# Performance work log

Hardware: AMD Instinct MI355X
Metric: run time of the kernel (lower is better)

The kernel has to match this reference:

```python
import jax, jax.numpy as jnp
import numpy as np

C = 256
E = C // 2  # embed_dim = in_channels / 2


def setup_inputs() -> dict:
    key = jax.random.key(0)
    ks = jax.random.split(key, 9)
    B, H, W = 8, 64, 64
    x = jax.random.normal(ks[0], (B, C, H, W), dtype=jnp.float32)
    s_in = 1.0 / np.sqrt(C)
    s_e = 1.0 / np.sqrt(E)
    wq = jax.random.uniform(ks[1], (E, C), jnp.float32, -s_in, s_in)
    bq = jax.random.uniform(ks[2], (E,), jnp.float32, -s_in, s_in)
    wk = jax.random.uniform(ks[3], (E, C), jnp.float32, -s_in, s_in)
    bk = jax.random.uniform(ks[4], (E,), jnp.float32, -s_in, s_in)
    wv = jax.random.uniform(ks[5], (E, C), jnp.float32, -s_in, s_in)
    bv = jax.random.uniform(ks[6], (E,), jnp.float32, -s_in, s_in)
    wo = jax.random.uniform(ks[7], (C, E), jnp.float32, -s_e, s_e)
    bo = jax.random.uniform(ks[8], (C,), jnp.float32, -s_e, s_e)
    return {"x": x, "wq": wq, "bq": bq, "wk": wk, "bk": bk,
            "wv": wv, "bv": bv, "wo": wo, "bo": bo}


def reference(x, wq, bq, wk, bk, wv, bv, wo, bo):
    B, Cc, H, W = x.shape
    N = H * W
    # flatten spatial: [B, N, C]; 1x1 conv == per-pixel linear over channels
    xf = x.reshape(B, Cc, N).transpose(0, 2, 1)
    q = jnp.einsum('bnc,ec->bne', xf, wq) + bq   # [B, N, E]
    k = jnp.einsum('bnc,ec->bne', xf, wk) + bk   # [B, N, E]
    v = jnp.einsum('bnc,ec->bne', xf, wv) + bv   # [B, N, E]
    attn_score = jnp.einsum('bne,bme->bnm', q, k)  # [B, N, N]
    attn_prob = jax.nn.softmax(attn_score, axis=-1)
    feat = jnp.einsum('bnm,bme->bne', attn_prob, v)  # [B, N, E]
    out = jnp.einsum('bne,ce->bnc', feat, wo) + bo   # expansion 1x1 conv
    out = out.transpose(0, 2, 1).reshape(B, Cc, H, W)
    return out + x
```

## Files before the change

### kernel.cpp

```cpp
#include <hip/hip_runtime.h>
#include <hip/hip_bf16.h>


typedef __attribute__((ext_vector_type(8))) short s16x8;
typedef __attribute__((ext_vector_type(4))) short s16x4;
typedef __attribute__((ext_vector_type(4))) float f32x4;

#define B_ 8
#define C_ 256
#define E_ 128
#define N_ 4096
#define SHIFT 15.0f

static __device__ __forceinline__ unsigned short f2bf(float f) {
    union { float f; unsigned int u; } v; v.f = f;
    return (unsigned short)((v.u + 0x7FFFu + ((v.u >> 16) & 1u)) >> 16);
}
static __device__ __forceinline__ float bf2f(unsigned short h) {
    union { unsigned int u; float f; } v; v.u = ((unsigned int)h) << 16;
    return v.f;
}

__global__ __launch_bounds__(256) void convert_w(
    const float* __restrict__ wq, const float* __restrict__ wk,
    const float* __restrict__ wv, const float* __restrict__ wo,
    unsigned short* __restrict__ wqb, unsigned short* __restrict__ wkb,
    unsigned short* __restrict__ wvb, unsigned short* __restrict__ wob)
{
    const int i = blockIdx.x * 256 + threadIdx.x;
    wqb[i] = f2bf(wq[i]);
    wkb[i] = f2bf(wk[i]);
    wvb[i] = f2bf(wv[i]);
    wob[i] = f2bf(wo[i]);
}

__global__ __launch_bounds__(256, 2) void qkv_kernel(
    const float* __restrict__ x,
    const unsigned short* __restrict__ wqb, const float* __restrict__ bq,
    const unsigned short* __restrict__ wkb, const float* __restrict__ bk,
    const unsigned short* __restrict__ wvb, const float* __restrict__ bv,
    unsigned short* __restrict__ Q, unsigned short* __restrict__ K,
    unsigned short* __restrict__ Vt)
{
    __shared__ unsigned short xs[64 * 264];

    const int tid = threadIdx.x;
    const int b  = blockIdx.x >> 6;
    const int n0 = (blockIdx.x & 63) << 6;

    {
        const int n  = tid & 63;
        const int c0 = tid >> 6;
        const float* xp = x + ((size_t)(b * C_) << 12) + n0 + n;
        for (int it = 0; it < 64; ++it) {
            const int c = it * 4 + c0;
            xs[n * 264 + c] = f2bf(xp[(size_t)c << 12]);
        }
    }
    __syncthreads();

    const int w = tid >> 6, l = tid & 63, hi = l >> 4, lx = l & 15;

    for (int idx = w; idx < 24; idx += 4) {
        const int out = idx >> 3;
        const int et  = idx & 7;
        const int e0  = et << 4;
        const unsigned short* W = (out == 0) ? wqb : (out == 1) ? wkb : wvb;
        const float* bias = (out == 0) ? bq : (out == 1) ? bk : bv;

        s16x8 af[8];
        const unsigned short* wp = W + (e0 + lx) * C_ + hi * 8;
#pragma unroll
        for (int ks = 0; ks < 8; ++ks) af[ks] = *(const s16x8*)(wp + ks * 32);

        float bi[4];
#pragma unroll
        for (int r = 0; r < 4; ++r) bi[r] = bias[e0 + hi * 4 + r];

#pragma unroll
        for (int nt = 0; nt < 4; ++nt) {
            f32x4 acc = {0.f, 0.f, 0.f, 0.f};
#pragma unroll
            for (int ks = 0; ks < 8; ++ks) {
                s16x8 xb = *(const s16x8*)&xs[(nt * 16 + lx) * 264 + ks * 32 + hi * 8];
                acc = __builtin_amdgcn_mfma_f32_16x16x32_bf16(af[ks], xb, acc, 0, 0, 0);
            }
            const int n = n0 + nt * 16 + lx;
            if (out < 2) {
                unsigned short* dst =
                    ((out == 0) ? Q : K) + ((size_t)(b * N_ + n) << 7) + e0 + hi * 4;
                s16x4 pk;
#pragma unroll
                for (int r = 0; r < 4; ++r) pk[r] = (short)f2bf(acc[r] + bi[r]);
                *(s16x4*)dst = pk;
            } else {
#pragma unroll
                for (int r = 0; r < 4; ++r)
                    Vt[((size_t)(b * E_ + e0 + hi * 4 + r) << 12) + n] =
                        f2bf(acc[r] + bi[r]);
            }
        }
    }
}

__global__ __launch_bounds__(256, 2) void attn_partial(
    const unsigned short* __restrict__ Q, const unsigned short* __restrict__ K,
    const unsigned short* __restrict__ Vt,
    unsigned short* __restrict__ featP, float* __restrict__ denomP)
{
    __shared__ unsigned short Ks[64 * 136];
    __shared__ unsigned short Vs[128 * 72];
    __shared__ unsigned short Ps[4][32 * 72];

    const int tid = threadIdx.x;
    const int b   = blockIdx.x & 7;
    const int idx = blockIdx.x >> 3;
    const int sl  = idx >> 5;
    const int qt  = idx & 31;
    const int w = tid >> 6, l = tid & 63, hi = l >> 4, lx = l & 15;
    const int q0 = qt * 128 + w * 32;

    s16x8 qA[2][4];
#pragma unroll
    for (int qf = 0; qf < 2; ++qf) {
        const unsigned short* qp =
            Q + ((size_t)(b * N_ + q0 + qf * 16 + lx) << 7) + hi * 8;
#pragma unroll
        for (int ks = 0; ks < 4; ++ks) qA[qf][ks] = *(const s16x8*)(qp + ks * 32);
    }

    f32x4 feat[2][8];
#pragma unroll
    for (int qf = 0; qf < 2; ++qf)
#pragma unroll
        for (int ef = 0; ef < 8; ++ef) feat[qf][ef] = (f32x4){0.f, 0.f, 0.f, 0.f};
    float dAcc[8];
#pragma unroll
    for (int i = 0; i < 8; ++i) dAcc[i] = 0.f;

    const unsigned short* Kg = K + ((size_t)(b * N_) << 7);
    const unsigned short* Vg = Vt + ((size_t)(b * E_) << 12);
    const int pswz_w = hi << 3;
    const int pswz_r = (lx & 12) << 1;

    for (int it = 0; it < 16; ++it) {
        const int kv0 = (sl << 10) + it * 64;
        __syncthreads();
#pragma unroll
        for (int i = 0; i < 4; ++i) {
            const int flat = tid + i * 256;
            const int row = flat >> 4, c16 = flat & 15;
            *(s16x8*)&Ks[row * 136 + c16 * 8] =
                *(const s16x8*)(Kg + (size_t)(kv0 + row) * 128 + c16 * 8);
        }
#pragma unroll
        for (int i = 0; i < 4; ++i) {
            const int flat = tid + i * 256;
            const int e = flat >> 3, c16 = flat & 7;
            *(s16x8*)&Vs[e * 72 + c16 * 8] =
                *(const s16x8*)(Vg + ((size_t)e << 12) + kv0 + c16 * 8);
        }
        __syncthreads();

        unsigned short* pw = &Ps[w][0];
#pragma unroll
        for (int kvf = 0; kvf < 4; ++kvf) {
            s16x8 kb[4];
#pragma unroll
            for (int ks = 0; ks < 4; ++ks)
                kb[ks] = *(const s16x8*)&Ks[(kvf * 16 + lx) * 136 + ks * 32 + hi * 8];
            const int pcol = (kvf * 16 + lx) ^ pswz_w;
#pragma unroll
            for (int qf = 0; qf < 2; ++qf) {
                f32x4 acc = {0.f, 0.f, 0.f, 0.f};
#pragma unroll
                for (int ks = 0; ks < 4; ++ks)
                    acc = __builtin_amdgcn_mfma_f32_16x16x32_bf16(qA[qf][ks], kb[ks], acc, 0, 0, 0);
#pragma unroll
                for (int r = 0; r < 4; ++r) {
                    float p = __expf(acc[r] - SHIFT);
                    dAcc[qf * 4 + r] += p;
                    pw[(qf * 16 + hi * 4 + r) * 72 + pcol] = f2bf(p);
                }
            }
        }
#pragma unroll
        for (int ks = 0; ks < 2; ++ks) {
            s16x8 pa[2];
#pragma unroll
            for (int qf = 0; qf < 2; ++qf)
                pa[qf] = *(const s16x8*)&pw[(qf * 16 + lx) * 72 +
                                            ((ks * 32 + hi * 8) ^ pswz_r)];
#pragma unroll
            for (int ef = 0; ef < 8; ++ef) {
                s16x8 vb = *(const s16x8*)&Vs[(ef * 16 + lx) * 72 + ks * 32 + hi * 8];
#pragma unroll
                for (int qf = 0; qf < 2; ++qf)
                    feat[qf][ef] = __builtin_amdgcn_mfma_f32_16x16x32_bf16(pa[qf], vb, feat[qf][ef], 0, 0, 0);
            }
        }
    }

#pragma unroll
    for (int i = 0; i < 8; ++i) {
        float v = dAcc[i];
        v += __shfl_xor(v, 1); v += __shfl_xor(v, 2);
        v += __shfl_xor(v, 4); v += __shfl_xor(v, 8);
        dAcc[i] = v;
    }
    const size_t qg = (size_t)((sl * 8 + b) * N_ + qt * 128 + w * 32);
    if (lx == 0) {
        float* dP = denomP + qg;
#pragma unroll
        for (int qf = 0; qf < 2; ++qf)
#pragma unroll
            for (int r = 0; r < 4; ++r)
                dP[qf * 16 + hi * 4 + r] = dAcc[qf * 4 + r];
    }
    unsigned short* fP = featP + (qg << 7);
#pragma unroll
    for (int qf = 0; qf < 2; ++qf)
#pragma unroll
        for (int ef = 0; ef < 8; ++ef)
#pragma unroll
            for (int r = 0; r < 4; ++r)
                fP[(qf * 16 + hi * 4 + r) * 128 + ef * 16 + lx] =
                    f2bf(feat[qf][ef][r]);
}

__global__ __launch_bounds__(256, 2) void combine_kernel(
    const unsigned short* __restrict__ featP, const float* __restrict__ denomP,
    const unsigned short* __restrict__ wob, const float* __restrict__ bo,
    const float* __restrict__ x, float* __restrict__ out)
{
    __shared__ unsigned short fs[64 * 136];

    const int tid = threadIdx.x;
    const int b  = blockIdx.x & 7;
    const int nt = blockIdx.x >> 3;

    {
        const int q = tid >> 2, eb = (tid & 3) * 32;
        const int n = nt * 64 + q;
        float den = 0.f;
#pragma unroll
        for (int s = 0; s < 4; ++s) den += denomP[(size_t)((s * 8 + b) * N_) + n];
        const float inv = 1.f / den;
#pragma unroll
        for (int e8 = 0; e8 < 4; ++e8) {
            float acc[8];
#pragma unroll
            for (int j = 0; j < 8; ++j) acc[j] = 0.f;
#pragma unroll
            for (int s = 0; s < 4; ++s) {
                s16x8 v = *(const s16x8*)(featP +
                    (((size_t)((s * 8 + b) * N_) + n) << 7) + eb + e8 * 8);
#pragma unroll
                for (int j = 0; j < 8; ++j) acc[j] += bf2f((unsigned short)v[j]);
            }
            s16x8 o;
#pragma unroll
            for (int j = 0; j < 8; ++j) o[j] = (short)f2bf(acc[j] * inv);
            *(s16x8*)&fs[q * 136 + eb + e8 * 8] = o;
        }
    }
    __syncthreads();

    const int w = tid >> 6, l = tid & 63, hi = l >> 4, lx = l & 15;

    s16x8 fa[4];
#pragma unroll
    for (int ks = 0; ks < 4; ++ks)
        fa[ks] = *(const s16x8*)&fs[(w * 16 + lx) * 136 + ks * 32 + hi * 8];

    const int n = nt * 64 + w * 16 + lx;
    const float* xb = x + ((size_t)(b * C_) << 12);
    float* ob = out + ((size_t)(b * C_) << 12);
#pragma unroll 1
    for (int ct = 0; ct < 16; ++ct) {
        const unsigned short* wp = wob + (ct * 16 + lx) * 128 + hi * 8;
        f32x4 acc = {0.f, 0.f, 0.f, 0.f};
#pragma unroll
        for (int ks = 0; ks < 4; ++ks) {
            s16x8 wb = *(const s16x8*)(wp + ks * 32);
            acc = __builtin_amdgcn_mfma_f32_16x16x32_bf16(wb, fa[ks], acc, 0, 0, 0);
        }
#pragma unroll
        for (int r = 0; r < 4; ++r) {
            const int c = ct * 16 + hi * 4 + r;
            const size_t off = ((size_t)c << 12) + n;
            ob[off] = acc[r] + bo[c] + xb[off];
        }
    }
}

extern "C" void kernel_launch(void* const* d_in, const int* in_sizes, int n_in,
                              void* d_out, int out_size, void* d_ws, size_t ws_size,
                              hipStream_t stream) {
    (void)in_sizes; (void)n_in; (void)out_size; (void)ws_size;
    const float* x  = (const float*)d_in[0];
    const float* wq = (const float*)d_in[1];
    const float* bq = (const float*)d_in[2];
    const float* wk = (const float*)d_in[3];
    const float* bk = (const float*)d_in[4];
    const float* wv = (const float*)d_in[5];
    const float* bv = (const float*)d_in[6];
    const float* wo = (const float*)d_in[7];
    const float* bo = (const float*)d_in[8];

    unsigned short* Q  = (unsigned short*)d_ws;
    unsigned short* K  = Q + (size_t)B_ * N_ * E_;
    unsigned short* Vt = K + (size_t)B_ * N_ * E_;
    unsigned short* featP = Vt + (size_t)B_ * N_ * E_;
    float* denomP = (float*)(featP + (size_t)4 * B_ * N_ * E_);
    unsigned short* wqb = (unsigned short*)(denomP + (size_t)4 * B_ * N_);
    unsigned short* wkb = wqb + E_ * C_;
    unsigned short* wvb = wkb + E_ * C_;
    unsigned short* wob = wvb + E_ * C_;

    convert_w<<<dim3(128), dim3(256), 0, stream>>>(
        wq, wk, wv, wo, wqb, wkb, wvb, wob);
    qkv_kernel<<<dim3(B_ * (N_ / 64)), dim3(256), 0, stream>>>(
        x, wqb, bq, wkb, bk, wvb, bv, Q, K, Vt);
    attn_partial<<<dim3(B_ * 32 * 4), dim3(256), 0, stream>>>(
        Q, K, Vt, featP, denomP);
    combine_kernel<<<dim3(B_ * 64), dim3(256), 0, stream>>>(
        featP, denomP, wob, bo, x, (float*)d_out);
}
```

Measured before the change: 143.7 us.

## Prefetch next KV tile into registers and halve KV split slices

The attention kernel now loads the next K/V tile from global memory into registers while computing on the current tile in shared memory, overlapping global latency with MFMA work. The number of KV slices is cut from 4 to 2, which halves the partial feat/denominator traffic and combine work but also halves the grid (512 blocks) and doubles per-block loop length. The XOR swizzle on the P scratch buffer is replaced by a padded stride of 76, changing the bank-conflict pattern. Register pressure rises from holding the prefetched tile.

```diff
diff --git a/kernel.cpp b/kernel.cpp
--- a/kernel.cpp
+++ b/kernel.cpp
@@ -10,6 +10,10 @@
 #define C_ 256
 #define E_ 128
 #define N_ 4096
+#define SLICES 2
+#define SLICE_KV (N_ / SLICES)
+#define NT (SLICE_KV / 64)
+#define PST 76
 #define SHIFT 15.0f
 
 static __device__ __forceinline__ unsigned short f2bf(float f) {
@@ -110,7 +114,7 @@
 {
     __shared__ unsigned short Ks[64 * 136];
     __shared__ unsigned short Vs[128 * 72];
-    __shared__ unsigned short Ps[4][32 * 72];
+    __shared__ unsigned short Ps[4][32 * PST];
 
     const int tid = threadIdx.x;
     const int b   = blockIdx.x & 7;
@@ -140,28 +144,32 @@
 
     const unsigned short* Kg = K + ((size_t)(b * N_) << 7);
     const unsigned short* Vg = Vt + ((size_t)(b * E_) << 12);
-    const int pswz_w = hi << 3;
-    const int pswz_r = (lx & 12) << 1;
-
-    for (int it = 0; it < 16; ++it) {
-        const int kv0 = (sl << 10) + it * 64;
-        __syncthreads();
-#pragma unroll
-        for (int i = 0; i < 4; ++i) {
-            const int flat = tid + i * 256;
-            const int row = flat >> 4, c16 = flat & 15;
-            *(s16x8*)&Ks[row * 136 + c16 * 8] =
-                *(const s16x8*)(Kg + (size_t)(kv0 + row) * 128 + c16 * 8);
-        }
-#pragma unroll
-        for (int i = 0; i < 4; ++i) {
-            const int flat = tid + i * 256;
-            const int e = flat >> 3, c16 = flat & 7;
-            *(s16x8*)&Vs[e * 72 + c16 * 8] =
-                *(const s16x8*)(Vg + ((size_t)e << 12) + kv0 + c16 * 8);
-        }
-        __syncthreads();
-
+    const int kvBase = sl * SLICE_KV;
+
+    const int kRow[4] = { (tid + 0) >> 4, (tid + 256) >> 4,
+                          (tid + 512) >> 4, (tid + 768) >> 4 };
+    const int kC16 = tid & 15;
+    const int vE[4]  = { (tid + 0) >> 3, (tid + 256) >> 3,
+                         (tid + 512) >> 3, (tid + 768) >> 3 };
+    const int vC16 = tid & 7;
+
+    auto loadTile = [&](int kv0, s16x8* nk, s16x8* nv) {
+#pragma unroll
+        for (int i = 0; i < 4; ++i)
+            nk[i] = *(const s16x8*)(Kg + (size_t)(kv0 + kRow[i]) * 128 + kC16 * 8);
+#pragma unroll
+        for (int i = 0; i < 4; ++i)
+            nv[i] = *(const s16x8*)(Vg + ((size_t)vE[i] << 12) + kv0 + vC16 * 8);
+    };
+    auto writeTile = [&](const s16x8* nk, const s16x8* nv) {
+#pragma unroll
+        for (int i = 0; i < 4; ++i)
+            *(s16x8*)&Ks[kRow[i] * 136 + kC16 * 8] = nk[i];
+#pragma unroll
+        for (int i = 0; i < 4; ++i)
+            *(s16x8*)&Vs[vE[i] * 72 + vC16 * 8] = nv[i];
+    };
+    auto compute = [&]() {
         unsigned short* pw = &Ps[w][0];
 #pragma unroll
         for (int kvf = 0; kvf < 4; ++kvf) {
@@ -169,7 +177,6 @@
 #pragma unroll
             for (int ks = 0; ks < 4; ++ks)
                 kb[ks] = *(const s16x8*)&Ks[(kvf * 16 + lx) * 136 + ks * 32 + hi * 8];
-            const int pcol = (kvf * 16 + lx) ^ pswz_w;
 #pragma unroll
             for (int qf = 0; qf < 2; ++qf) {
                 f32x4 acc = {0.f, 0.f, 0.f, 0.f};
@@ -180,7 +187,7 @@
                 for (int r = 0; r < 4; ++r) {
                     float p = __expf(acc[r] - SHIFT);
                     dAcc[qf * 4 + r] += p;
-                    pw[(qf * 16 + hi * 4 + r) * 72 + pcol] = f2bf(p);
+                    pw[(qf * 16 + hi * 4 + r) * PST + kvf * 16 + lx] = f2bf(p);
                 }
             }
         }
@@ -189,8 +196,7 @@
             s16x8 pa[2];
 #pragma unroll
             for (int qf = 0; qf < 2; ++qf)
-                pa[qf] = *(const s16x8*)&pw[(qf * 16 + lx) * 72 +
-                                            ((ks * 32 + hi * 8) ^ pswz_r)];
+                pa[qf] = *(const s16x8*)&pw[(qf * 16 + lx) * PST + ks * 32 + hi * 8];
 #pragma unroll
             for (int ef = 0; ef < 8; ++ef) {
                 s16x8 vb = *(const s16x8*)&Vs[(ef * 16 + lx) * 72 + ks * 32 + hi * 8];
@@ -199,7 +205,24 @@
                     feat[qf][ef] = __builtin_amdgcn_mfma_f32_16x16x32_bf16(pa[qf], vb, feat[qf][ef], 0, 0, 0);
             }
         }
-    }
+    };
+
+    {
+        s16x8 nk[4], nv[4];
+        loadTile(kvBase, nk, nv);
+        writeTile(nk, nv);
+    }
+    __syncthreads();
+
+    for (int it = 0; it < NT - 1; ++it) {
+        s16x8 nk[4], nv[4];
+        loadTile(kvBase + (it + 1) * 64, nk, nv);
+        compute();
+        __syncthreads();
+        writeTile(nk, nv);
+        __syncthreads();
+    }
+    compute();
 
 #pragma unroll
     for (int i = 0; i < 8; ++i) {
@@ -208,7 +231,7 @@
         v += __shfl_xor(v, 4); v += __shfl_xor(v, 8);
         dAcc[i] = v;
     }
-    const size_t qg = (size_t)((sl * 8 + b) * N_ + qt * 128 + w * 32);
+    const size_t qg = (size_t)((sl * 8 + b) * N_ + q0);
     if (lx == 0) {
         float* dP = denomP + qg;
 #pragma unroll
@@ -244,7 +267,8 @@
         const int n = nt * 64 + q;
         float den = 0.f;
 #pragma unroll
-        for (int s = 0; s < 4; ++s) den += denomP[(size_t)((s * 8 + b) * N_) + n];
+        for (int s = 0; s < SLICES; ++s)
+            den += denomP[(size_t)((s * 8 + b) * N_) + n];
         const float inv = 1.f / den;
 #pragma unroll
         for (int e8 = 0; e8 < 4; ++e8) {
@@ -252,7 +276,7 @@
 #pragma unroll
             for (int j = 0; j < 8; ++j) acc[j] = 0.f;
 #pragma unroll
-            for (int s = 0; s < 4; ++s) {
+            for (int s = 0; s < SLICES; ++s) {
                 s16x8 v = *(const s16x8*)(featP +
                     (((size_t)((s * 8 + b) * N_) + n) << 7) + eb + e8 * 8);
 #pragma unroll
@@ -312,8 +336,8 @@
     unsigned short* K  = Q + (size_t)B_ * N_ * E_;
     unsigned short* Vt = K + (size_t)B_ * N_ * E_;
     unsigned short* featP = Vt + (size_t)B_ * N_ * E_;
-    float* denomP = (float*)(featP + (size_t)4 * B_ * N_ * E_);
-    unsigned short* wqb = (unsigned short*)(denomP + (size_t)4 * B_ * N_);
+    float* denomP = (float*)(featP + (size_t)SLICES * B_ * N_ * E_);
+    unsigned short* wqb = (unsigned short*)(denomP + (size_t)SLICES * B_ * N_);
     unsigned short* wkb = wqb + E_ * C_;
     unsigned short* wvb = wkb + E_ * C_;
     unsigned short* wob = wvb + E_ * C_;
@@ -322,7 +346,7 @@
         wq, wk, wv, wo, wqb, wkb, wvb, wob);
     qkv_kernel<<<dim3(B_ * (N_ / 64)), dim3(256), 0, stream>>>(
         x, wqb, bq, wkb, bk, wvb, bv, Q, K, Vt);
-    attn_partial<<<dim3(B_ * 32 * 4), dim3(256), 0, stream>>>(
+    attn_partial<<<dim3(B_ * 32 * SLICES), dim3(256), 0, stream>>>(
         Q, K, Vt, featP, denomP);
     combine_kernel<<<dim3(B_ * 64), dim3(256), 0, stream>>>(
         featP, denomP, wob, bo, x, (float*)d_out);
```

New measurement: 168.7 us. +17.5%, slower.

## Read V directly from global memory and raise attention occupancy

Applied to the files above, without the earlier changes.

The attention kernel no longer stages V tiles in shared memory; each wave loads its V fragments straight from global memory inside the PV MFMA loop. Freeing that LDS lets launch bounds rise from 2 to 4 blocks per CU. The P buffer swizzle is replaced by a padded stride of 76, and the QK loop is reorganised to share each K fragment across both query fragments. In exchange, every wave issues its own global V loads, which relies on L2 hits and may expose load latency in the inner loop.

```diff
diff --git a/kernel.cpp b/kernel.cpp
--- a/kernel.cpp
+++ b/kernel.cpp
@@ -10,6 +10,10 @@
 #define C_ 256
 #define E_ 128
 #define N_ 4096
+#define SLICES 4
+#define SLICE_KV (N_ / SLICES)
+#define NTILES (SLICE_KV / 64)
+#define PST 76
 #define SHIFT 15.0f
 
 static __device__ __forceinline__ unsigned short f2bf(float f) {
@@ -103,14 +107,13 @@
     }
 }
 
-__global__ __launch_bounds__(256, 2) void attn_partial(
+__global__ __launch_bounds__(256, 4) void attn_partial(
     const unsigned short* __restrict__ Q, const unsigned short* __restrict__ K,
     const unsigned short* __restrict__ Vt,
     unsigned short* __restrict__ featP, float* __restrict__ denomP)
 {
-    __shared__ unsigned short Ks[64 * 136];
-    __shared__ unsigned short Vs[128 * 72];
-    __shared__ unsigned short Ps[4][32 * 72];
+    __shared__ unsigned short Kx[64 * 136];
+    __shared__ unsigned short Ps[4][32 * PST];
 
     const int tid = threadIdx.x;
     const int b   = blockIdx.x & 7;
@@ -140,63 +143,49 @@
 
     const unsigned short* Kg = K + ((size_t)(b * N_) << 7);
     const unsigned short* Vg = Vt + ((size_t)(b * E_) << 12);
-    const int pswz_w = hi << 3;
-    const int pswz_r = (lx & 12) << 1;
-
-    for (int it = 0; it < 16; ++it) {
-        const int kv0 = (sl << 10) + it * 64;
+    unsigned short* pw = &Ps[w][0];
+
+    for (int it = 0; it < NTILES; ++it) {
+        const int kv0 = sl * SLICE_KV + it * 64;
         __syncthreads();
 #pragma unroll
         for (int i = 0; i < 4; ++i) {
             const int flat = tid + i * 256;
             const int row = flat >> 4, c16 = flat & 15;
-            *(s16x8*)&Ks[row * 136 + c16 * 8] =
+            *(s16x8*)&Kx[row * 136 + c16 * 8] =
                 *(const s16x8*)(Kg + (size_t)(kv0 + row) * 128 + c16 * 8);
         }
-#pragma unroll
-        for (int i = 0; i < 4; ++i) {
-            const int flat = tid + i * 256;
-            const int e = flat >> 3, c16 = flat & 7;
-            *(s16x8*)&Vs[e * 72 + c16 * 8] =
-                *(const s16x8*)(Vg + ((size_t)e << 12) + kv0 + c16 * 8);
-        }
         __syncthreads();
 
-        unsigned short* pw = &Ps[w][0];
 #pragma unroll
         for (int kvf = 0; kvf < 4; ++kvf) {
-            s16x8 kb[4];
-#pragma unroll
-            for (int ks = 0; ks < 4; ++ks)
-                kb[ks] = *(const s16x8*)&Ks[(kvf * 16 + lx) * 136 + ks * 32 + hi * 8];
-            const int pcol = (kvf * 16 + lx) ^ pswz_w;
-#pragma unroll
-            for (int qf = 0; qf < 2; ++qf) {
-                f32x4 acc = {0.f, 0.f, 0.f, 0.f};
-#pragma unroll
-                for (int ks = 0; ks < 4; ++ks)
-                    acc = __builtin_amdgcn_mfma_f32_16x16x32_bf16(qA[qf][ks], kb[ks], acc, 0, 0, 0);
-#pragma unroll
-                for (int r = 0; r < 4; ++r) {
-                    float p = __expf(acc[r] - SHIFT);
-                    dAcc[qf * 4 + r] += p;
-                    pw[(qf * 16 + hi * 4 + r) * 72 + pcol] = f2bf(p);
-                }
+            f32x4 s0 = {0.f, 0.f, 0.f, 0.f}, s1 = {0.f, 0.f, 0.f, 0.f};
+#pragma unroll
+            for (int ks = 0; ks < 4; ++ks) {
+                s16x8 kb = *(const s16x8*)&Kx[(kvf * 16 + lx) * 136 + ks * 32 + hi * 8];
+                s0 = __builtin_amdgcn_mfma_f32_16x16x32_bf16(qA[0][ks], kb, s0, 0, 0, 0);
+                s1 = __builtin_amdgcn_mfma_f32_16x16x32_bf16(qA[1][ks], kb, s1, 0, 0, 0);
+            }
+#pragma unroll
+            for (int r = 0; r < 4; ++r) {
+                float p0 = __expf(s0[r] - SHIFT);
+                float p1 = __expf(s1[r] - SHIFT);
+                dAcc[r]     += p0;
+                dAcc[4 + r] += p1;
+                pw[(hi * 4 + r) * PST      + kvf * 16 + lx] = f2bf(p0);
+                pw[(16 + hi * 4 + r) * PST + kvf * 16 + lx] = f2bf(p1);
             }
         }
 #pragma unroll
         for (int ks = 0; ks < 2; ++ks) {
-            s16x8 pa[2];
-#pragma unroll
-            for (int qf = 0; qf < 2; ++qf)
-                pa[qf] = *(const s16x8*)&pw[(qf * 16 + lx) * 72 +
-                                            ((ks * 32 + hi * 8) ^ pswz_r)];
+            s16x8 pa0 = *(const s16x8*)&pw[(lx)      * PST + ks * 32 + hi * 8];
+            s16x8 pa1 = *(const s16x8*)&pw[(16 + lx) * PST + ks * 32 + hi * 8];
 #pragma unroll
             for (int ef = 0; ef < 8; ++ef) {
-                s16x8 vb = *(const s16x8*)&Vs[(ef * 16 + lx) * 72 + ks * 32 + hi * 8];
-#pragma unroll
-                for (int qf = 0; qf < 2; ++qf)
-                    feat[qf][ef] = __builtin_amdgcn_mfma_f32_16x16x32_bf16(pa[qf], vb, feat[qf][ef], 0, 0, 0);
+                s16x8 vb = *(const s16x8*)(Vg + ((size_t)(ef * 16 + lx) << 12)
+                                              + kv0 + ks * 32 + hi * 8);
+                feat[0][ef] = __builtin_amdgcn_mfma_f32_16x16x32_bf16(pa0, vb, feat[0][ef], 0, 0, 0);
+                feat[1][ef] = __builtin_amdgcn_mfma_f32_16x16x32_bf16(pa1, vb, feat[1][ef], 0, 0, 0);
             }
         }
     }
@@ -208,7 +197,7 @@
         v += __shfl_xor(v, 4); v += __shfl_xor(v, 8);
         dAcc[i] = v;
     }
-    const size_t qg = (size_t)((sl * 8 + b) * N_ + qt * 128 + w * 32);
+    const size_t qg = (size_t)((sl * 8 + b) * N_ + q0);
     if (lx == 0) {
         float* dP = denomP + qg;
 #pragma unroll
@@ -244,7 +233,8 @@
         const int n = nt * 64 + q;
         float den = 0.f;
 #pragma unroll
-        for (int s = 0; s < 4; ++s) den += denomP[(size_t)((s * 8 + b) * N_) + n];
+        for (int s = 0; s < SLICES; ++s)
+            den += denomP[(size_t)((s * 8 + b) * N_) + n];
         const float inv = 1.f / den;
 #pragma unroll
         for (int e8 = 0; e8 < 4; ++e8) {
@@ -252,7 +242,7 @@
 #pragma unroll
             for (int j = 0; j < 8; ++j) acc[j] = 0.f;
 #pragma unroll
-            for (int s = 0; s < 4; ++s) {
+            for (int s = 0; s < SLICES; ++s) {
                 s16x8 v = *(const s16x8*)(featP +
                     (((size_t)((s * 8 + b) * N_) + n) << 7) + eb + e8 * 8);
 #pragma unroll
@@ -312,8 +302,8 @@
     unsigned short* K  = Q + (size_t)B_ * N_ * E_;
     unsigned short* Vt = K + (size_t)B_ * N_ * E_;
     unsigned short* featP = Vt + (size_t)B_ * N_ * E_;
-    float* denomP = (float*)(featP + (size_t)4 * B_ * N_ * E_);
-    unsigned short* wqb = (unsigned short*)(denomP + (size_t)4 * B_ * N_);
+    float* denomP = (float*)(featP + (size_t)SLICES * B_ * N_ * E_);
+    unsigned short* wqb = (unsigned short*)(denomP + (size_t)SLICES * B_ * N_);
     unsigned short* wkb = wqb + E_ * C_;
     unsigned short* wvb = wkb + E_ * C_;
     unsigned short* wob = wvb + E_ * C_;
@@ -322,7 +312,7 @@
         wq, wk, wv, wo, wqb, wkb, wvb, wob);
     qkv_kernel<<<dim3(B_ * (N_ / 64)), dim3(256), 0, stream>>>(
         x, wqb, bq, wkb, bk, wvb, bv, Q, K, Vt);
-    attn_partial<<<dim3(B_ * 32 * 4), dim3(256), 0, stream>>>(
+    attn_partial<<<dim3(B_ * 32 * SLICES), dim3(256), 0, stream>>>(
         Q, K, Vt, featP, denomP);
     combine_kernel<<<dim3(B_ * 64), dim3(256), 0, stream>>>(
         featP, denomP, wob, bo, x, (float*)d_out);
```

After: 360.1 us. +150.6%, slower.
